# Kernel optimization log

Measured on AMD Instinct MI355X. Metric: run time of the kernel, lower is better.

## Reference

```python
import jax, jax.numpy as jnp
import numpy as np

# nuScenes-scale config: batch 2, 360x360 BEV grid (1440/4), 128 channels,
# 10 classes, 200 proposals, 3x3 NMS kernel, 40k occupied voxels per sample.
B, H, W_GRID, NUM_CLS, NUM_PROP, NMS_K = 2, 360, 360, 10, 200, 3
C = 128
N_PER_B = 40000
NEG_FILL = -1000000.0  # scatter_nd fill value from to_dense()


def _bev_pos():
    # replicates create_2D_grid: coord = (x_index_along_dim1, y_index_along_dim0)
    xs = jnp.arange(H, dtype=jnp.float32)
    ys = jnp.arange(W_GRID, dtype=jnp.float32)
    by, bx = jnp.meshgrid(xs, ys, indexing='ij')  # by[i,j]=i, bx[i,j]=j
    return jnp.stack([bx, by], axis=-1).reshape(-1, 2)  # [H*W, 2]


def setup_inputs() -> dict:
    key = jax.random.key(0)
    ks = jax.random.split(key, 10)
    # unique spatial locations per batch sample (sparse voxel coords)
    flats = [jax.random.permutation(ks[i], H * W_GRID)[:N_PER_B] for i in range(B)]
    flat = jnp.concatenate(flats)
    b = jnp.repeat(jnp.arange(B), N_PER_B)
    indices = jnp.stack([b, flat // W_GRID, flat % W_GRID], axis=1).astype(jnp.int32)
    features = jax.random.normal(ks[4], (B * N_PER_B, C), jnp.float32)
    # heatmap head (pointwise linears standing in for the submconv stack)
    W_hm1 = jax.random.normal(ks[5], (C, C), jnp.float32) * (2.0 / C) ** 0.5
    b_hm1 = jnp.zeros((C,), jnp.float32)
    W_hm2 = jax.random.normal(ks[6], (C, NUM_CLS), jnp.float32) * (2.0 / C) ** 0.5
    b_hm2 = jnp.full((NUM_CLS,), -2.19, jnp.float32)  # fc[-1].bias.fill_(-2.19)
    # class_encoding: nn.Conv1d(num_class, channels, 1)
    W_cls = jax.random.normal(ks[7], (C, NUM_CLS), jnp.float32) * 0.1
    b_cls = jnp.zeros((C,), jnp.float32)
    return dict(features=features, W_hm1=W_hm1, b_hm1=b_hm1, W_hm2=W_hm2,
                b_hm2=b_hm2, W_cls=W_cls, b_cls=b_cls, indices=indices)


def reference(features, W_hm1, b_hm1, W_hm2, b_hm2, W_cls, b_cls, indices):
    bidx, yi, xi = indices[:, 0], indices[:, 1], indices[:, 2]
    HW = H * W_GRID

    # --- x.dense(): scatter voxel features to dense BEV grid (zero fill) ---
    xd = jnp.zeros((B, H, W_GRID, C), features.dtype).at[bidx, yi, xi].set(features)
    x_flat = xd.reshape(B, HW, C).transpose(0, 2, 1)  # [B, C, HW]

    # --- heatmap head (per-voxel) then to_dense() with -1e6 fill ---
    hm = jax.nn.relu(features @ W_hm1 + b_hm1) @ W_hm2 + b_hm2  # [N, NUM_CLS]
    dense_hm = jnp.full((B, H, W_GRID, NUM_CLS), NEG_FILL, hm.dtype)
    dense_hm = dense_hm.at[bidx, yi, xi].set(hm).transpose(0, 3, 1, 2)  # [B,K,H,W]

    heat = jax.nn.sigmoid(dense_hm)  # detached in original

    # --- NMS-kernel peak extraction ---
    pad = NMS_K // 2
    inner = jax.lax.reduce_window(heat, -jnp.inf, jax.lax.max,
                                  (1, 1, NMS_K, NMS_K), (1, 1, 1, 1), 'VALID')
    local_max = jnp.zeros_like(heat).at[:, :, pad:H - pad, pad:W_GRID - pad].set(inner)
    # pedestrian (8) and traffic_cone (9): kernel size 1
    local_max = local_max.at[:, 8].set(heat[:, 8]).at[:, 9].set(heat[:, 9])
    heat = heat * (heat == local_max)
    heat_f = heat.reshape(B, NUM_CLS, HW)

    # --- top-k proposals over (class, location) ---
    _, top = jax.lax.top_k(heat_f.reshape(B, -1), NUM_PROP)  # [B, P]
    cls = top // HW
    idx = top % HW

    # --- gather proposal features + class encoding ---
    qf = jnp.take_along_axis(x_flat, jnp.broadcast_to(idx[:, None, :], (B, C, NUM_PROP)), axis=2)
    onehot = jax.nn.one_hot(cls, NUM_CLS, dtype=qf.dtype)  # [B, P, K]
    qf = qf + jnp.einsum('ck,bpk->bcp', W_cls, onehot) + b_cls[None, :, None]

    # --- proposal positions and heatmap scores ---
    query_pos = _bev_pos()[idx]  # [B, P, 2]
    qhs = jnp.take_along_axis(heat_f, jnp.broadcast_to(idx[:, None, :], (B, NUM_CLS, NUM_PROP)), axis=2)
    return qf, query_pos, qhs, cls
```

## Files before the change

kernel.cpp:

```cpp
#include <hip/hip_runtime.h>

#define HW 129600
#define WG 360
#define HG 360
#define NCLS 10
#define NPROP 200
#define CDIM 128
#define NROWS 80000
#define NB 2
#define NPB (NROWS / NB)
#define SEL_CAP 4096
#define HBINS 4096
#define RPB 64
#define PSTR 12
#define BPB 32
#define RPH 128
#define NBLK 313
#define REG 64

__device__ __forceinline__ void lds_cp16(float* l, const float* g) {
  __builtin_amdgcn_global_load_lds(
      (const __attribute__((address_space(1))) void*)g,
      (__attribute__((address_space(3))) void*)l, 16, 0, 0);
}

__global__ __launch_bounds__(256, 4) void k_head(
    const float* __restrict__ feat, const float* __restrict__ W1,
    const float* __restrict__ b1, const float* __restrict__ W2,
    const float* __restrict__ b2, const int* __restrict__ idxs,
    float* __restrict__ val_raw, int* __restrict__ rowmap,
    unsigned int* __restrict__ hist, int* __restrict__ cnts) {
  __shared__ __align__(16) float lds_w[2][16 * 128];
  __shared__ __align__(16) float lds_f[2][RPB * 16];
  const int tid = threadIdx.x;
  const int row0 = blockIdx.x * RPB;
  const int tc = tid & 31;
  const int tr = tid >> 5;
  const int wv = tid >> 6;
  const int lane = tid & 63;

  auto stage = [&](int kt, int nb) {
#pragma unroll
    for (int c = 0; c < 2; ++c) {
      const int off = (wv * 2 + c) * 256;
      lds_cp16(&lds_w[nb][off], W1 + kt * 2048 + off + lane * 4);
    }
    {
      const int off = wv * 256;
      const int fidx = off + lane * 4;
      const int r = fidx >> 4, kk = fidx & 15;
      lds_cp16(&lds_f[nb][off],
               feat + (size_t)(row0 + r) * CDIM + kt * 16 + kk);
    }
  };

  stage(0, 0);
  if (blockIdx.x == 0) {
    uint4* h4 = (uint4*)hist;
    for (int i = tid; i < (NB * HBINS) / 4; i += 256)
      h4[i] = make_uint4(0u, 0u, 0u, 0u);
    for (int i = tid; i < NB * NBLK; i += 256) cnts[i] = 0;
  }
  if (tid < RPB) {
    int row = row0 + tid;
    int bb = idxs[row * 3 + 0];
    int yy = idxs[row * 3 + 1];
    int xx = idxs[row * 3 + 2];
    rowmap[(size_t)bb * HW + yy * WG + xx] = row;
  }
  __syncthreads();

  float acc[8][4];
#pragma unroll
  for (int r = 0; r < 8; ++r)
#pragma unroll
    for (int c = 0; c < 4; ++c) acc[r][c] = 0.f;

  for (int kt = 0; kt < 8; ++kt) {
    const int cb = kt & 1;
    if (kt < 7) stage(kt + 1, cb ^ 1);
#pragma unroll
    for (int kg = 0; kg < 4; ++kg) {
      float4 w0 = *(const float4*)(&lds_w[cb][(kg * 4 + 0) * 128 + tc * 4]);
      float4 w1 = *(const float4*)(&lds_w[cb][(kg * 4 + 1) * 128 + tc * 4]);
      float4 w2 = *(const float4*)(&lds_w[cb][(kg * 4 + 2) * 128 + tc * 4]);
      float4 w3 = *(const float4*)(&lds_w[cb][(kg * 4 + 3) * 128 + tc * 4]);
#pragma unroll
      for (int r = 0; r < 8; ++r) {
        float4 fv = *(const float4*)(&lds_f[cb][(tr * 8 + r) * 16 + kg * 4]);
        acc[r][0] = fmaf(fv.x, w0.x, acc[r][0]);
        acc[r][0] = fmaf(fv.y, w1.x, acc[r][0]);
        acc[r][0] = fmaf(fv.z, w2.x, acc[r][0]);
        acc[r][0] = fmaf(fv.w, w3.x, acc[r][0]);
        acc[r][1] = fmaf(fv.x, w0.y, acc[r][1]);
        acc[r][1] = fmaf(fv.y, w1.y, acc[r][1]);
        acc[r][1] = fmaf(fv.z, w2.y, acc[r][1]);
        acc[r][1] = fmaf(fv.w, w3.y, acc[r][1]);
        acc[r][2] = fmaf(fv.x, w0.z, acc[r][2]);
        acc[r][2] = fmaf(fv.y, w1.z, acc[r][2]);
        acc[r][2] = fmaf(fv.z, w2.z, acc[r][2]);
        acc[r][2] = fmaf(fv.w, w3.z, acc[r][2]);
        acc[r][3] = fmaf(fv.x, w0.w, acc[r][3]);
        acc[r][3] = fmaf(fv.y, w1.w, acc[r][3]);
        acc[r][3] = fmaf(fv.z, w2.w, acc[r][3]);
        acc[r][3] = fmaf(fv.w, w3.w, acc[r][3]);
      }
    }
    __syncthreads();
  }

  float* w2t = &lds_f[0][0];
  for (int i = tid; i < CDIM * NCLS; i += 256) {
    int k = i / NCLS, j = i - k * NCLS;
    w2t[j * 128 + k] = W2[i];
  }
  __syncthreads();

  float* hbuf = &lds_w[0][0];
  float4 b1v = *(const float4*)(b1 + tc * 4);
#pragma unroll
  for (int half = 0; half < 2; ++half) {
    if ((tr >> 2) == half) {
      int ltr = tr & 3;
#pragma unroll
      for (int r = 0; r < 8; ++r) {
        float4 h;
        h.x = fmaxf(acc[r][0] + b1v.x, 0.f);
        h.y = fmaxf(acc[r][1] + b1v.y, 0.f);
        h.z = fmaxf(acc[r][2] + b1v.z, 0.f);
        h.w = fmaxf(acc[r][3] + b1v.w, 0.f);
        *(float4*)(hbuf + (ltr * 8 + r) * 128 + tc * 4) = h;
      }
    }
    __syncthreads();
    for (int o = tid; o < 32 * NCLS; o += 256) {
      int r = o / NCLS, j = o - r * NCLS;
      float s = b2[j];
      for (int i4 = 0; i4 < 32; ++i4) {
        int k4 = (i4 + tid) & 31;
        float4 hv = *(const float4*)(hbuf + r * 128 + k4 * 4);
        float4 wv2 = *(const float4*)(w2t + j * 128 + k4 * 4);
        s = fmaf(hv.x, wv2.x, s);
        s = fmaf(hv.y, wv2.y, s);
        s = fmaf(hv.z, wv2.z, s);
        s = fmaf(hv.w, wv2.w, s);
      }
      float heat = 1.0f / (1.0f + expf(-s));
      int gr = half * 32 + r;
      val_raw[(size_t)(row0 + gr) * PSTR + j] = heat;
    }
    __syncthreads();
  }
}

__global__ __launch_bounds__(1024) void k_hist(
    const float* __restrict__ val_raw, const int* __restrict__ idxs,
    const int* __restrict__ rowmap, float* __restrict__ val,
    unsigned int* __restrict__ hist) {
  __shared__ unsigned int lh[NB * HBINS];
  const int tid = threadIdx.x;
  uint4* l4 = (uint4*)lh;
  l4[tid] = make_uint4(0u, 0u, 0u, 0u);
  l4[tid + 1024] = make_uint4(0u, 0u, 0u, 0u);
  __syncthreads();

  const int g = tid >> 3;
  const int n = tid & 7;
  const int row = blockIdx.x * RPH + g;
  const int bb = (row >= NPB) ? 1 : 0;
  const int y = idxs[row * 3 + 1];
  const int x = idxs[row * 3 + 2];
  const int pos = y * WG + x;
  const bool interior = (y > 0 && y < HG - 1 && x > 0 && x < WG - 1);
  const int dy = (n < 2) ? 0 : ((n < 5) ? -1 : 1);
  const int dx = (n < 2) ? (n * 2 - 1) : ((n < 5) ? (n - 3) : (n - 6));

  int nrow = -1;
  if (interior) nrow = rowmap[(size_t)bb * HW + pos + dy * WG + dx];
  const bool inb = ((unsigned)nrow < NROWS) && ((nrow >= NPB) == (bb == 1));
  const int safe = inb ? nrow : 0;
  const int y2 = idxs[safe * 3 + 1];
  const int x2 = idxs[safe * 3 + 2];
  const bool ok = inb && (y2 == y + dy) && (x2 == x + dx);
  float4 a = *(const float4*)(val_raw + (size_t)safe * PSTR);
  float4 b = *(const float4*)(val_raw + (size_t)safe * PSTR + 4);
  if (!ok) {
    a.x = a.y = a.z = a.w = 0.f;
    b.x = b.y = b.z = b.w = 0.f;
  }
#pragma unroll
  for (int m = 1; m <= 4; m <<= 1) {
    a.x = fmaxf(a.x, __shfl_xor(a.x, m));
    a.y = fmaxf(a.y, __shfl_xor(a.y, m));
    a.z = fmaxf(a.z, __shfl_xor(a.z, m));
    a.w = fmaxf(a.w, __shfl_xor(a.w, m));
    b.x = fmaxf(b.x, __shfl_xor(b.x, m));
    b.y = fmaxf(b.y, __shfl_xor(b.y, m));
    b.z = fmaxf(b.z, __shfl_xor(b.z, m));
    b.w = fmaxf(b.w, __shfl_xor(b.w, m));
  }
  if (n == 0) {
    const float* cbase = val_raw + (size_t)row * PSTR;
    float4 c0 = *(const float4*)(cbase + 0);
    float4 c1 = *(const float4*)(cbase + 4);
    float2 c89 = *(const float2*)(cbase + 8);
    float v[10];
    if (interior) {
      v[0] = (c0.x >= a.x) ? c0.x : 0.f;
      v[1] = (c0.y >= a.y) ? c0.y : 0.f;
      v[2] = (c0.z >= a.z) ? c0.z : 0.f;
      v[3] = (c0.w >= a.w) ? c0.w : 0.f;
      v[4] = (c1.x >= b.x) ? c1.x : 0.f;
      v[5] = (c1.y >= b.y) ? c1.y : 0.f;
      v[6] = (c1.z >= b.z) ? c1.z : 0.f;
      v[7] = (c1.w >= b.w) ? c1.w : 0.f;
    } else {
      v[0] = v[1] = v[2] = v[3] = v[4] = v[5] = v[6] = v[7] = 0.f;
    }
    v[8] = c89.x;
    v[9] = c89.y;
    float4 s0 = {v[0], v[1], v[2], v[3]};
    float4 s1 = {v[4], v[5], v[6], v[7]};
    float4 s2 = {v[8], v[9], 0.f, 0.f};
    *(float4*)(val + (size_t)row * PSTR + 0) = s0;
    *(float4*)(val + (size_t)row * PSTR + 4) = s1;
    *(float4*)(val + (size_t)row * PSTR + 8) = s2;
    unsigned int* lhb = lh + bb * HBINS;
#pragma unroll
    for (int c = 0; c < 10; ++c) {
      if (v[c] > 0.f) atomicAdd(&lhb[__float_as_uint(v[c]) >> 18], 1u);
    }
  }
  __syncthreads();
  for (int i = tid; i < (NB * HBINS) / 4; i += 1024) {
    uint4 q = l4[i];
    if (q.x) atomicAdd(&hist[i * 4 + 0], q.x);
    if (q.y) atomicAdd(&hist[i * 4 + 1], q.y);
    if (q.z) atomicAdd(&hist[i * 4 + 2], q.z);
    if (q.w) atomicAdd(&hist[i * 4 + 3], q.w);
  }
}

__global__ __launch_bounds__(256) void k_collect(
    const float* __restrict__ val, const int* __restrict__ idxs,
    const unsigned int* __restrict__ hist, unsigned long long* __restrict__ sel,
    int* __restrict__ cnts) {
  __shared__ unsigned int coarse[256];
  __shared__ unsigned int fine16[16];
  __shared__ int sT[2];
  __shared__ int sCi[2];
  __shared__ int lcnt[2];
  const int tid = threadIdx.x;
  if (tid < 2) lcnt[tid] = 0;
  for (int bb = 0; bb < NB; ++bb) {
    const unsigned int* h = hist + (size_t)bb * HBINS;
    const uint4* h4 = (const uint4*)(h + tid * 16);
    unsigned int s = 0;
#pragma unroll
    for (int i = 0; i < 4; ++i) {
      uint4 q = h4[i];
      s += q.x + q.y + q.z + q.w;
    }
    if (tid == 0) {
      sCi[bb] = -1;
      sT[bb] = 0;
    }
    coarse[tid] = s;
    __syncthreads();
#pragma unroll
    for (int off = 1; off < 256; off <<= 1) {
      unsigned int vv = (tid + off < 256) ? coarse[tid + off] : 0u;
      __syncthreads();
      coarse[tid] += vv;
      __syncthreads();
    }
    if (coarse[tid] >= NPROP) atomicMax(&sCi[bb], tid);
    __syncthreads();
    const int ci = sCi[bb];
    if (ci >= 0) {
      if (tid < 16) fine16[tid] = h[ci * 16 + tid];
      __syncthreads();
      if (tid == 0) {
        unsigned int cum = (ci + 1 < 256) ? coarse[ci + 1] : 0u;
        int t = 15;
        for (; t > 0; --t) {
          unsigned int c = fine16[t];
          if (cum + c >= NPROP) break;
          cum += c;
        }
        sT[bb] = ci * 16 + t;
      }
    }
    __syncthreads();
  }
  const int row = blockIdx.x * 256 + tid;
  const bool valid = row < NROWS;
  const int bb = (valid && row >= NPB) ? 1 : 0;
  const int T = sT[bb];
  float v[12];
  int pos = 0;
  if (valid) {
    *(float4*)(v + 0) = *(const float4*)(val + (size_t)row * PSTR + 0);
    *(float4*)(v + 4) = *(const float4*)(val + (size_t)row * PSTR + 4);
    *(float4*)(v + 8) = *(const float4*)(val + (size_t)row * PSTR + 8);
    pos = idxs[row * 3 + 1] * WG + idxs[row * 3 + 2];
  }
#pragma unroll
  for (int cl = 0; cl < 10; ++cl) {
    float vv = valid ? v[cl] : 0.f;
    unsigned int bits = __float_as_uint(vv);
    bool pred = (vv > 0.f) && ((int)(bits >> 18) >= T);
    if (pred) {
      int ls = atomicAdd(&lcnt[bb], 1);
      if (ls < REG) {
        unsigned int gidx = (unsigned int)cl * HW + (unsigned int)pos;
        unsigned long long key =
            ((unsigned long long)bits << 32) | (unsigned long long)(~gidx);
        sel[((size_t)bb * NBLK + blockIdx.x) * REG + ls] = key;
      }
    }
  }
  __syncthreads();
  if (tid < 2) {
    int c = lcnt[tid];
    cnts[tid * NBLK + blockIdx.x] = (c < REG) ? c : REG;
  }
}

__global__ __launch_bounds__(256) void k_final(
    const unsigned long long* __restrict__ sel, const int* __restrict__ cnts,
    const float* __restrict__ val, const int* __restrict__ rowmap,
    const float* __restrict__ feat, const float* __restrict__ Wc,
    const float* __restrict__ bc, float* __restrict__ out) {
  __shared__ unsigned long long sk[SEL_CAP];
  __shared__ unsigned long long winners[NPROP];
  __shared__ int wcls[NPROP];
  __shared__ int wrow[NPROP];
  __shared__ int spref[NBLK + 1];
  const int b = blockIdx.x / BPB;
  const int part = blockIdx.x % BPB;
  const int tid = threadIdx.x;
  if (tid == 0) {
    int acc = 0;
    for (int i = 0; i < NBLK; ++i) {
      spref[i] = acc;
      acc += cnts[b * NBLK + i];
    }
    spref[NBLK] = acc;
  }
  __syncthreads();
  int M = spref[NBLK];
  if (M > SEL_CAP) M = SEL_CAP;
  for (int i = tid; i < NBLK; i += 256) {
    int base = spref[i];
    int c = spref[i + 1] - base;
    const unsigned long long* src = sel + ((size_t)b * NBLK + i) * REG;
    for (int j = 0; j < c; ++j) {
      int d = base + j;
      if (d < SEL_CAP) sk[d] = src[j];
    }
  }
  __syncthreads();
  for (int i = tid; i < M; i += 256) {
    unsigned long long key = sk[i];
    int rank = 0;
    for (int j = 0; j < M; ++j) rank += (sk[j] > key) ? 1 : 0;
    if (rank < NPROP) winners[rank] = key;
  }
  __syncthreads();
  if (tid < NPROP) {
    unsigned long long key = winners[tid];
    unsigned int gidx = ~((unsigned int)(key & 0xFFFFFFFFull));
    int cls = (int)(gidx / HW);
    int pos = (int)(gidx - (unsigned int)cls * HW);
    wcls[tid] = cls;
    wrow[tid] = rowmap[(size_t)b * HW + pos];
    if (part == 0) {
      int y = pos / WG, x = pos - y * WG;
      out[51200 + ((size_t)b * NPROP + tid) * 2 + 0] = (float)x;
      out[51200 + ((size_t)b * NPROP + tid) * 2 + 1] = (float)y;
      out[56000 + b * NPROP + tid] = (float)cls;
    }
  }
  __syncthreads();
  for (int o = part * 256 + tid; o < NCLS * NPROP; o += BPB * 256) {
    int j = o / NPROP, pp = o - j * NPROP;
    out[52000 + (size_t)b * NCLS * NPROP + o] = val[(size_t)wrow[pp] * PSTR + j];
  }
  for (int o = part * 256 + tid; o < CDIM * NPROP; o += BPB * 256) {
    int c = o / NPROP, pp = o - c * NPROP;
    out[(size_t)b * CDIM * NPROP + o] =
        feat[(size_t)wrow[pp] * CDIM + c] + Wc[c * NCLS + wcls[pp]] + bc[c];
  }
}

extern "C" void kernel_launch(void* const* d_in, const int* in_sizes, int n_in,
                              void* d_out, int out_size, void* d_ws,
                              size_t ws_size, hipStream_t stream) {
  const float* feat = (const float*)d_in[0];
  const float* W1 = (const float*)d_in[1];
  const float* b1 = (const float*)d_in[2];
  const float* W2 = (const float*)d_in[3];
  const float* b2 = (const float*)d_in[4];
  const float* Wc = (const float*)d_in[5];
  const float* bc = (const float*)d_in[6];
  const int* idxs = (const int*)d_in[7];
  float* out = (float*)d_out;

  char* ws = (char*)d_ws;
  unsigned int* hist = (unsigned int*)(ws + 0);
  int* rowmap = (int*)(ws + 32768);
  int* cnts = (int*)(ws + 1069568);
  unsigned long long* sel = (unsigned long long*)(ws + 1072080);
  float* val_raw = (float*)(ws + 1392592);
  float* val = (float*)(ws + 5232592);

  k_head<<<NROWS / RPB, 256, 0, stream>>>(feat, W1, b1, W2, b2, idxs, val_raw,
                                          rowmap, hist, cnts);
  k_hist<<<NROWS / RPH, 1024, 0, stream>>>(val_raw, idxs, rowmap, val, hist);
  k_collect<<<NBLK, 256, 0, stream>>>(val, idxs, hist, sel, cnts);
  k_final<<<NB * BPB, 256, 0, stream>>>(sel, cnts, val, rowmap, feat, Wc, bc,
                                        out);
}
```

Baseline: 206.9 us.

## Fuse hist, collect and final kernels into one persistent kernel with grid barriers

Replaces the three tail kernels (local-max/histogram, threshold collect, top-k final gather) with a single persistent kernel of 256 blocks that separates phases with atomic-counter grid barriers. The aim is to remove two kernel launch boundaries and their drain/refill gaps. The tiles per block and the selection region size change to match. Correctness depends on all 256 blocks of 1024 threads being co-resident, which is not guaranteed by a normal launch. The barrier spin and single-thread serial prefix add latency in exchange.

```diff
diff --git a/kernel.cpp b/kernel.cpp
--- a/kernel.cpp
+++ b/kernel.cpp
@@ -13,10 +13,12 @@
 #define HBINS 4096
 #define RPB 64
 #define PSTR 12
-#define BPB 32
-#define RPH 128
-#define NBLK 313
-#define REG 64
+#define TGRID 256
+#define TBLK 1024
+#define NTILE 625
+#define CTILE 79
+#define REG 96
+#define DPART 128
 
 __device__ __forceinline__ void lds_cp16(float* l, const float* g) {
   __builtin_amdgcn_global_load_lds(
@@ -24,12 +26,24 @@
       (__attribute__((address_space(3))) void*)l, 16, 0, 0);
 }
 
+__device__ __forceinline__ void gbar(int* ctr) {
+  __syncthreads();
+  if (threadIdx.x == 0) {
+    __threadfence();
+    atomicAdd(ctr, 1);
+    while (atomicAdd(ctr, 0) < TGRID) __builtin_amdgcn_s_sleep(8);
+  }
+  __syncthreads();
+  __threadfence();
+}
+
 __global__ __launch_bounds__(256, 4) void k_head(
     const float* __restrict__ feat, const float* __restrict__ W1,
     const float* __restrict__ b1, const float* __restrict__ W2,
     const float* __restrict__ b2, const int* __restrict__ idxs,
     float* __restrict__ val_raw, int* __restrict__ rowmap,
-    unsigned int* __restrict__ hist, int* __restrict__ cnts) {
+    unsigned int* __restrict__ hist, int* __restrict__ cnts,
+    int* __restrict__ bar) {
   __shared__ __align__(16) float lds_w[2][16 * 128];
   __shared__ __align__(16) float lds_f[2][RPB * 16];
   const int tid = threadIdx.x;
@@ -59,7 +73,8 @@
     uint4* h4 = (uint4*)hist;
     for (int i = tid; i < (NB * HBINS) / 4; i += 256)
       h4[i] = make_uint4(0u, 0u, 0u, 0u);
-    for (int i = tid; i < NB * NBLK; i += 256) cnts[i] = 0;
+    for (int i = tid; i < NB * CTILE; i += 256) cnts[i] = 0;
+    if (tid < 2) bar[tid] = 0;
   }
   if (tid < RPB) {
     int row = row0 + tid;
@@ -153,132 +168,143 @@
   }
 }
 
-__global__ __launch_bounds__(1024) void k_hist(
+__global__ __launch_bounds__(TBLK) void k_tail(
     const float* __restrict__ val_raw, const int* __restrict__ idxs,
     const int* __restrict__ rowmap, float* __restrict__ val,
-    unsigned int* __restrict__ hist) {
-  __shared__ unsigned int lh[NB * HBINS];
+    unsigned int* __restrict__ hist, unsigned long long* __restrict__ sel,
+    int* __restrict__ cnts, int* __restrict__ bar,
+    const float* __restrict__ feat, const float* __restrict__ Wc,
+    const float* __restrict__ bc, float* __restrict__ out) {
+  __shared__ __align__(16) unsigned int lh[NB * HBINS];
+  __shared__ unsigned int coarse[256];
+  __shared__ unsigned int fine16[16];
+  __shared__ int sT[NB], sCi[NB], lcnt[NB];
+  __shared__ int spref[CTILE + 1];
+  __shared__ unsigned long long winners[NPROP];
+  __shared__ int wcls[NPROP], wrow[NPROP];
+
   const int tid = threadIdx.x;
-  uint4* l4 = (uint4*)lh;
-  l4[tid] = make_uint4(0u, 0u, 0u, 0u);
-  l4[tid + 1024] = make_uint4(0u, 0u, 0u, 0u);
-  __syncthreads();
-
+  const int blk = blockIdx.x;
+
+  {
+    uint4* l4 = (uint4*)lh;
+    l4[tid] = make_uint4(0u, 0u, 0u, 0u);
+    l4[tid + TBLK] = make_uint4(0u, 0u, 0u, 0u);
+  }
+  __syncthreads();
   const int g = tid >> 3;
   const int n = tid & 7;
-  const int row = blockIdx.x * RPH + g;
-  const int bb = (row >= NPB) ? 1 : 0;
-  const int y = idxs[row * 3 + 1];
-  const int x = idxs[row * 3 + 2];
-  const int pos = y * WG + x;
-  const bool interior = (y > 0 && y < HG - 1 && x > 0 && x < WG - 1);
   const int dy = (n < 2) ? 0 : ((n < 5) ? -1 : 1);
   const int dx = (n < 2) ? (n * 2 - 1) : ((n < 5) ? (n - 3) : (n - 6));
 
-  int nrow = -1;
-  if (interior) nrow = rowmap[(size_t)bb * HW + pos + dy * WG + dx];
-  const bool inb = ((unsigned)nrow < NROWS) && ((nrow >= NPB) == (bb == 1));
-  const int safe = inb ? nrow : 0;
-  const int y2 = idxs[safe * 3 + 1];
-  const int x2 = idxs[safe * 3 + 2];
-  const bool ok = inb && (y2 == y + dy) && (x2 == x + dx);
-  float4 a = *(const float4*)(val_raw + (size_t)safe * PSTR);
-  float4 b = *(const float4*)(val_raw + (size_t)safe * PSTR + 4);
-  if (!ok) {
-    a.x = a.y = a.z = a.w = 0.f;
-    b.x = b.y = b.z = b.w = 0.f;
-  }
-#pragma unroll
-  for (int m = 1; m <= 4; m <<= 1) {
-    a.x = fmaxf(a.x, __shfl_xor(a.x, m));
-    a.y = fmaxf(a.y, __shfl_xor(a.y, m));
-    a.z = fmaxf(a.z, __shfl_xor(a.z, m));
-    a.w = fmaxf(a.w, __shfl_xor(a.w, m));
-    b.x = fmaxf(b.x, __shfl_xor(b.x, m));
-    b.y = fmaxf(b.y, __shfl_xor(b.y, m));
-    b.z = fmaxf(b.z, __shfl_xor(b.z, m));
-    b.w = fmaxf(b.w, __shfl_xor(b.w, m));
-  }
-  if (n == 0) {
-    const float* cbase = val_raw + (size_t)row * PSTR;
-    float4 c0 = *(const float4*)(cbase + 0);
-    float4 c1 = *(const float4*)(cbase + 4);
-    float2 c89 = *(const float2*)(cbase + 8);
-    float v[10];
-    if (interior) {
-      v[0] = (c0.x >= a.x) ? c0.x : 0.f;
-      v[1] = (c0.y >= a.y) ? c0.y : 0.f;
-      v[2] = (c0.z >= a.z) ? c0.z : 0.f;
-      v[3] = (c0.w >= a.w) ? c0.w : 0.f;
-      v[4] = (c1.x >= b.x) ? c1.x : 0.f;
-      v[5] = (c1.y >= b.y) ? c1.y : 0.f;
-      v[6] = (c1.z >= b.z) ? c1.z : 0.f;
-      v[7] = (c1.w >= b.w) ? c1.w : 0.f;
-    } else {
-      v[0] = v[1] = v[2] = v[3] = v[4] = v[5] = v[6] = v[7] = 0.f;
-    }
-    v[8] = c89.x;
-    v[9] = c89.y;
-    float4 s0 = {v[0], v[1], v[2], v[3]};
-    float4 s1 = {v[4], v[5], v[6], v[7]};
-    float4 s2 = {v[8], v[9], 0.f, 0.f};
-    *(float4*)(val + (size_t)row * PSTR + 0) = s0;
-    *(float4*)(val + (size_t)row * PSTR + 4) = s1;
-    *(float4*)(val + (size_t)row * PSTR + 8) = s2;
-    unsigned int* lhb = lh + bb * HBINS;
-#pragma unroll
-    for (int c = 0; c < 10; ++c) {
-      if (v[c] > 0.f) atomicAdd(&lhb[__float_as_uint(v[c]) >> 18], 1u);
-    }
-  }
-  __syncthreads();
-  for (int i = tid; i < (NB * HBINS) / 4; i += 1024) {
-    uint4 q = l4[i];
-    if (q.x) atomicAdd(&hist[i * 4 + 0], q.x);
-    if (q.y) atomicAdd(&hist[i * 4 + 1], q.y);
-    if (q.z) atomicAdd(&hist[i * 4 + 2], q.z);
-    if (q.w) atomicAdd(&hist[i * 4 + 3], q.w);
-  }
-}
-
-__global__ __launch_bounds__(256) void k_collect(
-    const float* __restrict__ val, const int* __restrict__ idxs,
-    const unsigned int* __restrict__ hist, unsigned long long* __restrict__ sel,
-    int* __restrict__ cnts) {
-  __shared__ unsigned int coarse[256];
-  __shared__ unsigned int fine16[16];
-  __shared__ int sT[2];
-  __shared__ int sCi[2];
-  __shared__ int lcnt[2];
-  const int tid = threadIdx.x;
-  if (tid < 2) lcnt[tid] = 0;
+  for (int t = blk; t < NTILE; t += TGRID) {
+    const int row = t * 128 + g;
+    const int bb = (row >= NPB) ? 1 : 0;
+    const int y = idxs[row * 3 + 1];
+    const int x = idxs[row * 3 + 2];
+    const int pos = y * WG + x;
+    const bool interior = (y > 0 && y < HG - 1 && x > 0 && x < WG - 1);
+    int nrow = -1;
+    if (interior) nrow = rowmap[(size_t)bb * HW + pos + dy * WG + dx];
+    const bool inb = ((unsigned)nrow < NROWS) && ((nrow >= NPB) == (bb == 1));
+    const int safe = inb ? nrow : 0;
+    const int y2 = idxs[safe * 3 + 1];
+    const int x2 = idxs[safe * 3 + 2];
+    const bool ok = inb && (y2 == y + dy) && (x2 == x + dx);
+    float4 a = *(const float4*)(val_raw + (size_t)safe * PSTR);
+    float4 b = *(const float4*)(val_raw + (size_t)safe * PSTR + 4);
+    if (!ok) {
+      a.x = a.y = a.z = a.w = 0.f;
+      b.x = b.y = b.z = b.w = 0.f;
+    }
+#pragma unroll
+    for (int m = 1; m <= 4; m <<= 1) {
+      a.x = fmaxf(a.x, __shfl_xor(a.x, m));
+      a.y = fmaxf(a.y, __shfl_xor(a.y, m));
+      a.z = fmaxf(a.z, __shfl_xor(a.z, m));
+      a.w = fmaxf(a.w, __shfl_xor(a.w, m));
+      b.x = fmaxf(b.x, __shfl_xor(b.x, m));
+      b.y = fmaxf(b.y, __shfl_xor(b.y, m));
+      b.z = fmaxf(b.z, __shfl_xor(b.z, m));
+      b.w = fmaxf(b.w, __shfl_xor(b.w, m));
+    }
+    if (n == 0) {
+      const float* cbase = val_raw + (size_t)row * PSTR;
+      float4 c0 = *(const float4*)(cbase + 0);
+      float4 c1 = *(const float4*)(cbase + 4);
+      float2 c89 = *(const float2*)(cbase + 8);
+      float v[10];
+      if (interior) {
+        v[0] = (c0.x >= a.x) ? c0.x : 0.f;
+        v[1] = (c0.y >= a.y) ? c0.y : 0.f;
+        v[2] = (c0.z >= a.z) ? c0.z : 0.f;
+        v[3] = (c0.w >= a.w) ? c0.w : 0.f;
+        v[4] = (c1.x >= b.x) ? c1.x : 0.f;
+        v[5] = (c1.y >= b.y) ? c1.y : 0.f;
+        v[6] = (c1.z >= b.z) ? c1.z : 0.f;
+        v[7] = (c1.w >= b.w) ? c1.w : 0.f;
+      } else {
+        v[0] = v[1] = v[2] = v[3] = v[4] = v[5] = v[6] = v[7] = 0.f;
+      }
+      v[8] = c89.x;
+      v[9] = c89.y;
+      float4 s0 = {v[0], v[1], v[2], v[3]};
+      float4 s1 = {v[4], v[5], v[6], v[7]};
+      float4 s2 = {v[8], v[9], 0.f, 0.f};
+      *(float4*)(val + (size_t)row * PSTR + 0) = s0;
+      *(float4*)(val + (size_t)row * PSTR + 4) = s1;
+      *(float4*)(val + (size_t)row * PSTR + 8) = s2;
+      unsigned int* lhb = lh + bb * HBINS;
+#pragma unroll
+      for (int c = 0; c < 10; ++c) {
+        if (v[c] > 0.f) atomicAdd(&lhb[__float_as_uint(v[c]) >> 18], 1u);
+      }
+    }
+  }
+  __syncthreads();
+  {
+    uint4* l4 = (uint4*)lh;
+    for (int i = tid; i < (NB * HBINS) / 4; i += TBLK) {
+      uint4 q = l4[i];
+      if (q.x) atomicAdd(&hist[i * 4 + 0], q.x);
+      if (q.y) atomicAdd(&hist[i * 4 + 1], q.y);
+      if (q.z) atomicAdd(&hist[i * 4 + 2], q.z);
+      if (q.w) atomicAdd(&hist[i * 4 + 3], q.w);
+    }
+  }
+
+  gbar(&bar[0]);
+
   for (int bb = 0; bb < NB; ++bb) {
-    const unsigned int* h = hist + (size_t)bb * HBINS;
-    const uint4* h4 = (const uint4*)(h + tid * 16);
-    unsigned int s = 0;
-#pragma unroll
-    for (int i = 0; i < 4; ++i) {
-      uint4 q = h4[i];
-      s += q.x + q.y + q.z + q.w;
-    }
     if (tid == 0) {
       sCi[bb] = -1;
       sT[bb] = 0;
     }
-    coarse[tid] = s;
+    if (tid < 256) {
+      const unsigned int* h = hist + (size_t)bb * HBINS;
+      const uint4* h4 = (const uint4*)(h + tid * 16);
+      unsigned int s = 0;
+#pragma unroll
+      for (int i = 0; i < 4; ++i) {
+        uint4 q = h4[i];
+        s += q.x + q.y + q.z + q.w;
+      }
+      coarse[tid] = s;
+    }
     __syncthreads();
 #pragma unroll
     for (int off = 1; off < 256; off <<= 1) {
-      unsigned int vv = (tid + off < 256) ? coarse[tid + off] : 0u;
+      unsigned int vv = 0;
+      if (tid < 256 && tid + off < 256) vv = coarse[tid + off];
       __syncthreads();
-      coarse[tid] += vv;
+      if (tid < 256) coarse[tid] += vv;
       __syncthreads();
     }
-    if (coarse[tid] >= NPROP) atomicMax(&sCi[bb], tid);
+    if (tid < 256 && coarse[tid] >= NPROP) atomicMax(&sCi[bb], tid);
     __syncthreads();
     const int ci = sCi[bb];
     if (ci >= 0) {
-      if (tid < 16) fine16[tid] = h[ci * 16 + tid];
+      if (tid < 16) fine16[tid] = hist[(size_t)bb * HBINS + ci * 16 + tid];
       __syncthreads();
       if (tid == 0) {
         unsigned int cum = (ci + 1 < 256) ? coarse[ci + 1] : 0u;
@@ -293,75 +319,71 @@
     }
     __syncthreads();
   }
-  const int row = blockIdx.x * 256 + tid;
-  const bool valid = row < NROWS;
-  const int bb = (valid && row >= NPB) ? 1 : 0;
-  const int T = sT[bb];
-  float v[12];
-  int pos = 0;
-  if (valid) {
-    *(float4*)(v + 0) = *(const float4*)(val + (size_t)row * PSTR + 0);
-    *(float4*)(v + 4) = *(const float4*)(val + (size_t)row * PSTR + 4);
-    *(float4*)(v + 8) = *(const float4*)(val + (size_t)row * PSTR + 8);
-    pos = idxs[row * 3 + 1] * WG + idxs[row * 3 + 2];
-  }
-#pragma unroll
-  for (int cl = 0; cl < 10; ++cl) {
-    float vv = valid ? v[cl] : 0.f;
-    unsigned int bits = __float_as_uint(vv);
-    bool pred = (vv > 0.f) && ((int)(bits >> 18) >= T);
-    if (pred) {
-      int ls = atomicAdd(&lcnt[bb], 1);
-      if (ls < REG) {
-        unsigned int gidx = (unsigned int)cl * HW + (unsigned int)pos;
-        unsigned long long key =
-            ((unsigned long long)bits << 32) | (unsigned long long)(~gidx);
-        sel[((size_t)bb * NBLK + blockIdx.x) * REG + ls] = key;
-      }
-    }
-  }
-  __syncthreads();
-  if (tid < 2) {
-    int c = lcnt[tid];
-    cnts[tid * NBLK + blockIdx.x] = (c < REG) ? c : REG;
-  }
-}
-
-__global__ __launch_bounds__(256) void k_final(
-    const unsigned long long* __restrict__ sel, const int* __restrict__ cnts,
-    const float* __restrict__ val, const int* __restrict__ rowmap,
-    const float* __restrict__ feat, const float* __restrict__ Wc,
-    const float* __restrict__ bc, float* __restrict__ out) {
-  __shared__ unsigned long long sk[SEL_CAP];
-  __shared__ unsigned long long winners[NPROP];
-  __shared__ int wcls[NPROP];
-  __shared__ int wrow[NPROP];
-  __shared__ int spref[NBLK + 1];
-  const int b = blockIdx.x / BPB;
-  const int part = blockIdx.x % BPB;
-  const int tid = threadIdx.x;
+
+  if (blk < CTILE) {
+    if (tid < NB) lcnt[tid] = 0;
+    __syncthreads();
+    const int row = blk * TBLK + tid;
+    const bool valid = row < NROWS;
+    const int bb = (valid && row >= NPB) ? 1 : 0;
+    const int T = sT[bb];
+    float v[12];
+    int pos = 0;
+    if (valid) {
+      *(float4*)(v + 0) = *(const float4*)(val + (size_t)row * PSTR + 0);
+      *(float4*)(v + 4) = *(const float4*)(val + (size_t)row * PSTR + 4);
+      *(float4*)(v + 8) = *(const float4*)(val + (size_t)row * PSTR + 8);
+      pos = idxs[row * 3 + 1] * WG + idxs[row * 3 + 2];
+    }
+#pragma unroll
+    for (int cl = 0; cl < 10; ++cl) {
+      float vv = valid ? v[cl] : 0.f;
+      unsigned int bits = __float_as_uint(vv);
+      bool pred = (vv > 0.f) && ((int)(bits >> 18) >= T);
+      if (pred) {
+        int ls = atomicAdd(&lcnt[bb], 1);
+        if (ls < REG) {
+          unsigned int gidx = (unsigned int)cl * HW + (unsigned int)pos;
+          unsigned long long key =
+              ((unsigned long long)bits << 32) | (unsigned long long)(~gidx);
+          sel[((size_t)bb * CTILE + blk) * REG + ls] = key;
+        }
+      }
+    }
+    __syncthreads();
+    if (tid < NB) {
+      int c = lcnt[tid];
+      cnts[tid * CTILE + blk] = (c < REG) ? c : REG;
+    }
+  }
+
+  gbar(&bar[1]);
+
+  const int b = blk / DPART;
+  const int part = blk % DPART;
   if (tid == 0) {
     int acc = 0;
-    for (int i = 0; i < NBLK; ++i) {
+    for (int i = 0; i < CTILE; ++i) {
       spref[i] = acc;
-      acc += cnts[b * NBLK + i];
-    }
-    spref[NBLK] = acc;
-  }
-  __syncthreads();
-  int M = spref[NBLK];
+      acc += cnts[b * CTILE + i];
+    }
+    spref[CTILE] = acc;
+  }
+  __syncthreads();
+  int M = spref[CTILE];
   if (M > SEL_CAP) M = SEL_CAP;
-  for (int i = tid; i < NBLK; i += 256) {
-    int base = spref[i];
-    int c = spref[i + 1] - base;
-    const unsigned long long* src = sel + ((size_t)b * NBLK + i) * REG;
+  unsigned long long* sk = (unsigned long long*)lh;
+  if (tid < CTILE) {
+    int base = spref[tid];
+    int c = spref[tid + 1] - base;
+    const unsigned long long* src = sel + ((size_t)b * CTILE + tid) * REG;
     for (int j = 0; j < c; ++j) {
       int d = base + j;
       if (d < SEL_CAP) sk[d] = src[j];
     }
   }
   __syncthreads();
-  for (int i = tid; i < M; i += 256) {
+  for (int i = tid; i < M; i += TBLK) {
     unsigned long long key = sk[i];
     int rank = 0;
     for (int j = 0; j < M; ++j) rank += (sk[j] > key) ? 1 : 0;
@@ -383,11 +405,12 @@
     }
   }
   __syncthreads();
-  for (int o = part * 256 + tid; o < NCLS * NPROP; o += BPB * 256) {
+  const int w = part * TBLK + tid;
+  for (int o = w; o < NCLS * NPROP; o += DPART * TBLK) {
     int j = o / NPROP, pp = o - j * NPROP;
     out[52000 + (size_t)b * NCLS * NPROP + o] = val[(size_t)wrow[pp] * PSTR + j];
   }
-  for (int o = part * 256 + tid; o < CDIM * NPROP; o += BPB * 256) {
+  for (int o = w; o < CDIM * NPROP; o += DPART * TBLK) {
     int c = o / NPROP, pp = o - c * NPROP;
     out[(size_t)b * CDIM * NPROP + o] =
         feat[(size_t)wrow[pp] * CDIM + c] + Wc[c * NCLS + wcls[pp]] + bc[c];
@@ -411,14 +434,13 @@
   unsigned int* hist = (unsigned int*)(ws + 0);
   int* rowmap = (int*)(ws + 32768);
   int* cnts = (int*)(ws + 1069568);
-  unsigned long long* sel = (unsigned long long*)(ws + 1072080);
-  float* val_raw = (float*)(ws + 1392592);
-  float* val = (float*)(ws + 5232592);
+  int* bar = (int*)(ws + 1070208);
+  unsigned long long* sel = (unsigned long long*)(ws + 1070224);
+  float* val_raw = (float*)(ws + 1191568);
+  float* val = (float*)(ws + 5031568);
 
   k_head<<<NROWS / RPB, 256, 0, stream>>>(feat, W1, b1, W2, b2, idxs, val_raw,
-                                          rowmap, hist, cnts);
-  k_hist<<<NROWS / RPH, 1024, 0, stream>>>(val_raw, idxs, rowmap, val, hist);
-  k_collect<<<NBLK, 256, 0, stream>>>(val, idxs, hist, sel, cnts);
-  k_final<<<NB * BPB, 256, 0, stream>>>(sel, cnts, val, rowmap, feat, Wc, bc,
-                                        out);
+                                          rowmap, hist, cnts, bar);
+  k_tail<<<TGRID, TBLK, 0, stream>>>(val_raw, idxs, rowmap, val, hist, sel,
+                                     cnts, bar, feat, Wc, bc, out);
 }
```

Result: slower. 311.7 us (+50.6%).
